# Performance work log

Measured on AMD Instinct MI355X. Metric: run time of the kernel, lower is better.

## Reference

```python
import jax, jax.numpy as jnp
import numpy as np

T, C, O, N = 131072, 512, 512, 1024


def setup_inputs() -> dict:
    key = jax.random.key(0)
    k1, k2, k3, k4, k5 = jax.random.split(key, 5)
    x = jax.random.normal(k1, (T, C), dtype=jnp.float32)
    segment_ids = jnp.sort(jax.random.randint(k2, (T,), 0, N)).astype(jnp.int64)
    # proj_func: Linear(C, O); score_func: Linear(C, 1)
    Wp = jax.random.normal(k3, (C, O), dtype=jnp.float32) / np.sqrt(C)
    bp = jnp.zeros((O,), dtype=jnp.float32)
    ws = jax.random.normal(k4, (C,), dtype=jnp.float32) / np.sqrt(C)
    bs = jnp.zeros((), dtype=jnp.float32)
    return {"x": x, "Wp": Wp, "bp": bp, "ws": ws, "bs": bs,
            "segment_ids": segment_ids, "num_segments": N}


def reference(x, Wp, bp, ws, bs, segment_ids, num_segments):
    # proj_x = Linear(x): [T, O]
    proj_x = x @ Wp + bp
    # score = Linear(x) squeezed to [T]
    score = x @ ws + bs
    # segment-wise numerically stable softmax over ragged segments
    seg_max = jax.ops.segment_max(score, segment_ids, num_segments=num_segments)
    seg_max = jnp.where(jnp.isfinite(seg_max), seg_max, 0.0)  # empty segments
    e = jnp.exp(score - seg_max[segment_ids])
    denom = jax.ops.segment_sum(e, segment_ids, num_segments=num_segments)
    w = e / denom[segment_ids]  # [T]
    # per-segment weighted sum of projected features -> [N, O]
    out = jax.ops.segment_sum(proj_x * w[:, None], segment_ids,
                              num_segments=num_segments)
    return out
```

## Files before the change

### kernel.cpp

```cpp
#include <hip/hip_runtime.h>
#include <hip/hip_bf16.h>
#include <cstdint>
#include <cstddef>

#define CC 512
#define OO 512
#define NN 1024
#define QPARTS 8
#define TB 4

__global__ void seg_bounds_kernel(const int* __restrict__ sid,
                                  int* __restrict__ seg_start,
                                  int T, int N) {
    int t = blockIdx.x * blockDim.x + threadIdx.x;
    if (t >= T) return;
    int s  = sid[t];
    int sp = (t == 0) ? -1 : sid[t - 1];
    for (int n = sp + 1; n <= s; ++n) seg_start[n] = t;
    if (t == T - 1) {
        for (int n = s + 1; n <= N; ++n) seg_start[n] = T;
    }
}

__device__ __forceinline__ float dot4(const float4 a, const float4 b) {
    return a.x * b.x + a.y * b.y + a.z * b.z + a.w * b.w;
}

__global__ __launch_bounds__(64) void seg_pool_partial(
    const float* __restrict__ x,
    const float* __restrict__ ws_g,
    const float* __restrict__ bs_g,
    const int*   __restrict__ seg_start,
    float*       __restrict__ pacc,
    float2*      __restrict__ pml)
{
    const int g = blockIdx.x;
    const int n = g >> 3;
    const int q = g & 7;
    const int s = seg_start[n];
    const int e = seg_start[n + 1];
    const int len = e - s;
    const int tb = s + (len * q) / QPARTS;
    const int te = s + (len * (q + 1)) / QPARTS;
    const int lane = threadIdx.x;
    const int c0 = lane * 4;

    const float4 w0 = *reinterpret_cast<const float4*>(ws_g + c0);
    const float4 w1 = *reinterpret_cast<const float4*>(ws_g + 256 + c0);
    const float  bsv = bs_g[0];

    float m = -INFINITY, l = 0.f;
    float4 a0 = make_float4(0.f, 0.f, 0.f, 0.f);
    float4 a1 = make_float4(0.f, 0.f, 0.f, 0.f);

    float4 A0[TB], A1[TB], B0[TB], B1[TB];

    auto LOADF = [&](float4 (&b0)[TB], float4 (&b1)[TB], const int t0) {
        #pragma unroll
        for (int j = 0; j < TB; ++j) {
            const int t = t0 + j;
            if (t < te) {
                const float* p = x + (size_t)t * CC;
                b0[j] = *reinterpret_cast<const float4*>(p + c0);
                b1[j] = *reinterpret_cast<const float4*>(p + 256 + c0);
            } else {
                b0[j] = make_float4(0.f, 0.f, 0.f, 0.f);
                b1[j] = make_float4(0.f, 0.f, 0.f, 0.f);
            }
        }
    };

    auto COMP = [&](float4 (&b0)[TB], float4 (&b1)[TB], const int t0) {
        float sc[TB];
        #pragma unroll
        for (int j = 0; j < TB; ++j) {
            float p = dot4(b0[j], w0) + dot4(b1[j], w1);
            #pragma unroll
            for (int off = 32; off >= 1; off >>= 1)
                p += __shfl_xor(p, off, 64);
            sc[j] = p + bsv;
        }
        float mc = -INFINITY;
        #pragma unroll
        for (int j = 0; j < TB; ++j)
            if (t0 + j < te) mc = fmaxf(mc, sc[j]);
        if (mc > m) {
            const float scale = (m == -INFINITY) ? 0.f : __expf(m - mc);
            l *= scale;
            a0.x *= scale; a0.y *= scale; a0.z *= scale; a0.w *= scale;
            a1.x *= scale; a1.y *= scale; a1.z *= scale; a1.w *= scale;
            m = mc;
        }
        #pragma unroll
        for (int j = 0; j < TB; ++j) {
            if (t0 + j < te) {
                const float wj = __expf(sc[j] - m);
                l += wj;
                a0.x += wj * b0[j].x; a0.y += wj * b0[j].y;
                a0.z += wj * b0[j].z; a0.w += wj * b0[j].w;
                a1.x += wj * b1[j].x; a1.y += wj * b1[j].y;
                a1.z += wj * b1[j].z; a1.w += wj * b1[j].w;
            }
        }
    };

    LOADF(A0, A1, tb);
    for (int t0 = tb; t0 < te; t0 += 2 * TB) {
        LOADF(B0, B1, t0 + TB);
        COMP(A0, A1, t0);
        LOADF(A0, A1, t0 + 2 * TB);
        COMP(B0, B1, t0 + TB);
    }

    float* pa = pacc + (size_t)g * CC;
    *reinterpret_cast<float4*>(pa + c0)       = a0;
    *reinterpret_cast<float4*>(pa + 256 + c0) = a1;
    if (lane == 0) pml[g] = make_float2(m, l);
}

__global__ __launch_bounds__(64) void seg_combine(
    const float*  __restrict__ pacc,
    const float2* __restrict__ pml,
    float*        __restrict__ y)
{
    const int n = blockIdx.x;
    const int lane = threadIdx.x;
    const int c0 = lane * 4;
    float* yp = y + (size_t)n * CC;

    float mq[QPARTS];
    float lq[QPARTS];
    float newm = -INFINITY;
    #pragma unroll
    for (int q = 0; q < QPARTS; ++q) {
        const float2 ml = pml[n * QPARTS + q];
        mq[q] = ml.x; lq[q] = ml.y;
        newm = fmaxf(newm, ml.x);
    }

    float4 o0 = make_float4(0.f, 0.f, 0.f, 0.f);
    float4 o1 = make_float4(0.f, 0.f, 0.f, 0.f);

    if (newm == -INFINITY) {
        *reinterpret_cast<float4*>(yp + c0)       = o0;
        *reinterpret_cast<float4*>(yp + 256 + c0) = o1;
        return;
    }

    float L = 0.f;
    #pragma unroll
    for (int q = 0; q < QPARTS; ++q) {
        const float wq = __expf(mq[q] - newm);
        L += wq * lq[q];
        const float* pa = pacc + (size_t)(n * QPARTS + q) * CC;
        const float4 p0 = *reinterpret_cast<const float4*>(pa + c0);
        const float4 p1 = *reinterpret_cast<const float4*>(pa + 256 + c0);
        o0.x += wq * p0.x; o0.y += wq * p0.y; o0.z += wq * p0.z; o0.w += wq * p0.w;
        o1.x += wq * p1.x; o1.y += wq * p1.y; o1.z += wq * p1.z; o1.w += wq * p1.w;
    }
    const float inv = 1.f / L;
    o0.x *= inv; o0.y *= inv; o0.z *= inv; o0.w *= inv;
    o1.x *= inv; o1.y *= inv; o1.z *= inv; o1.w *= inv;
    *reinterpret_cast<float4*>(yp + c0)       = o0;
    *reinterpret_cast<float4*>(yp + 256 + c0) = o1;
}

__global__ __launch_bounds__(256) void proj_kernel(
    float*       __restrict__ out,
    const float* __restrict__ Wp,
    const float* __restrict__ bp,
    const int*   __restrict__ seg_start)
{
    const int n0  = blockIdx.x * 4;
    const int tid = threadIdx.x;

    __shared__ float ylds[4][CC];
    {
        const float* src = out + (size_t)n0 * CC;
        for (int idx = tid; idx < 4 * CC / 4; idx += 256)
            reinterpret_cast<float4*>(&ylds[0][0])[idx] =
                reinterpret_cast<const float4*>(src)[idx];
    }
    __syncthreads();

    const int o0 = tid;
    const int o1 = tid + 256;
    float acc[4][2] = {};

    for (int k = 0; k < CC; k += 4) {
        float4 yv[4];
        #pragma unroll
        for (int r = 0; r < 4; ++r)
            yv[r] = *reinterpret_cast<const float4*>(&ylds[r][k]);
        #pragma unroll
        for (int kk = 0; kk < 4; ++kk) {
            const float w0 = Wp[(size_t)(k + kk) * OO + o0];
            const float w1 = Wp[(size_t)(k + kk) * OO + o1];
            #pragma unroll
            for (int r = 0; r < 4; ++r) {
                const float yval = reinterpret_cast<const float*>(&yv[r])[kk];
                acc[r][0] += yval * w0;
                acc[r][1] += yval * w1;
            }
        }
    }

    #pragma unroll
    for (int r = 0; r < 4; ++r) {
        const int n = n0 + r;
        const bool nonempty = seg_start[n + 1] > seg_start[n];
        const float b0 = nonempty ? bp[o0] : 0.f;
        const float b1 = nonempty ? bp[o1] : 0.f;
        out[(size_t)n * OO + o0] = acc[r][0] + b0;
        out[(size_t)n * OO + o1] = acc[r][1] + b1;
    }
}

extern "C" void kernel_launch(void* const* d_in, const int* in_sizes, int n_in,
                              void* d_out, int out_size, void* d_ws, size_t ws_size,
                              hipStream_t stream) {
    const float* x    = (const float*)d_in[0];
    const float* Wp   = (const float*)d_in[1];
    const float* bp   = (const float*)d_in[2];
    const float* wsv  = (const float*)d_in[3];
    const float* bs   = (const float*)d_in[4];
    const int*   sid  = (const int*)d_in[5];
    const int T = in_sizes[5];
    const int N = NN;

    int*    seg_start = (int*)d_ws;
    float*  pacc      = (float*)((char*)d_ws + 8192);
    float2* pml       = (float2*)((char*)d_ws + 8192 +
                                  (size_t)N * QPARTS * CC * sizeof(float));
    float*  out       = (float*)d_out;

    seg_bounds_kernel<<<(T + 255) / 256, 256, 0, stream>>>(sid, seg_start, T, N);
    seg_pool_partial<<<N * QPARTS, 64, 0, stream>>>(x, wsv, bs, seg_start, pacc, pml);
    seg_combine<<<N, 64, 0, stream>>>(pacc, pml, out);
    proj_kernel<<<N / 4, 256, 0, stream>>>(out, Wp, bp, seg_start);
}
```

Measured before the change: 92.05 us.

## Halve segment split count, use nontemporal loads and branchless aligned main loop

Each segment is now split into 4 partial blocks instead of 8, which halves the partial-accumulator traffic and the combine work. Split boundaries are aligned to multiples of 8 tokens, so the double-buffered main loop needs no per-token bounds checks and a separate tail loop handles leftovers. The streaming loads of x use nontemporal hints, and the online-softmax rescale becomes branchless using ext_vector float4 arithmetic. The cost is fewer blocks in flight (4096 single-wave blocks), which may reduce latency hiding on a memory-bound scan of a 256MB input.

```diff
diff --git a/kernel.cpp b/kernel.cpp
--- a/kernel.cpp
+++ b/kernel.cpp
@@ -6,8 +6,9 @@
 #define CC 512
 #define OO 512
 #define NN 1024
-#define QPARTS 8
-#define TB 4
+#define QP 4
+
+typedef float f4 __attribute__((ext_vector_type(4)));
 
 __global__ void seg_bounds_kernel(const int* __restrict__ sid,
                                   int* __restrict__ seg_start,
@@ -22,8 +23,15 @@
     }
 }
 
-__device__ __forceinline__ float dot4(const float4 a, const float4 b) {
+__device__ __forceinline__ float dot4(const f4 a, const f4 b) {
     return a.x * b.x + a.y * b.y + a.z * b.z + a.w * b.w;
+}
+
+__device__ __forceinline__ float wave_sum(float p) {
+    #pragma unroll
+    for (int off = 32; off >= 1; off >>= 1)
+        p += __shfl_xor(p, off, 64);
+    return p;
 }
 
 __global__ __launch_bounds__(64) void seg_pool_partial(
@@ -35,86 +43,113 @@
     float2*      __restrict__ pml)
 {
     const int g = blockIdx.x;
-    const int n = g >> 3;
-    const int q = g & 7;
+    const int n = g >> 2;
+    const int q = g & 3;
     const int s = seg_start[n];
     const int e = seg_start[n + 1];
     const int len = e - s;
-    const int tb = s + (len * q) / QPARTS;
-    const int te = s + (len * (q + 1)) / QPARTS;
+    const int tb = s + (((len * q) >> 2) & ~7);
+    const int te = (q == 3) ? e : (s + (((len * (q + 1)) >> 2) & ~7));
     const int lane = threadIdx.x;
     const int c0 = lane * 4;
 
-    const float4 w0 = *reinterpret_cast<const float4*>(ws_g + c0);
-    const float4 w1 = *reinterpret_cast<const float4*>(ws_g + 256 + c0);
-    const float  bsv = bs_g[0];
+    const f4 w0 = *reinterpret_cast<const f4*>(ws_g + c0);
+    const f4 w1 = *reinterpret_cast<const f4*>(ws_g + 256 + c0);
+    const float bsv = bs_g[0];
 
     float m = -INFINITY, l = 0.f;
-    float4 a0 = make_float4(0.f, 0.f, 0.f, 0.f);
-    float4 a1 = make_float4(0.f, 0.f, 0.f, 0.f);
-
-    float4 A0[TB], A1[TB], B0[TB], B1[TB];
-
-    auto LOADF = [&](float4 (&b0)[TB], float4 (&b1)[TB], const int t0) {
-        #pragma unroll
-        for (int j = 0; j < TB; ++j) {
-            const int t = t0 + j;
-            if (t < te) {
-                const float* p = x + (size_t)t * CC;
-                b0[j] = *reinterpret_cast<const float4*>(p + c0);
-                b1[j] = *reinterpret_cast<const float4*>(p + 256 + c0);
-            } else {
-                b0[j] = make_float4(0.f, 0.f, 0.f, 0.f);
-                b1[j] = make_float4(0.f, 0.f, 0.f, 0.f);
-            }
+    f4 a0 = {0.f, 0.f, 0.f, 0.f};
+    f4 a1 = {0.f, 0.f, 0.f, 0.f};
+
+    const int nTok  = te - tb;
+    const int nIter = nTok >> 3;
+
+    f4 A0[4], A1[4], B0[4], B1[4];
+
+    auto LOAD4 = [&](f4 (&b0)[4], f4 (&b1)[4], const float* p) {
+        #pragma unroll
+        for (int j = 0; j < 4; ++j) {
+            const float* r = p + (size_t)j * CC;
+            b0[j] = __builtin_nontemporal_load(
+                        reinterpret_cast<const f4*>(r + c0));
+            b1[j] = __builtin_nontemporal_load(
+                        reinterpret_cast<const f4*>(r + 256 + c0));
         }
     };
 
-    auto COMP = [&](float4 (&b0)[TB], float4 (&b1)[TB], const int t0) {
-        float sc[TB];
-        #pragma unroll
-        for (int j = 0; j < TB; ++j) {
-            float p = dot4(b0[j], w0) + dot4(b1[j], w1);
-            #pragma unroll
-            for (int off = 32; off >= 1; off >>= 1)
-                p += __shfl_xor(p, off, 64);
-            sc[j] = p + bsv;
-        }
-        float mc = -INFINITY;
-        #pragma unroll
-        for (int j = 0; j < TB; ++j)
-            if (t0 + j < te) mc = fmaxf(mc, sc[j]);
-        if (mc > m) {
-            const float scale = (m == -INFINITY) ? 0.f : __expf(m - mc);
-            l *= scale;
-            a0.x *= scale; a0.y *= scale; a0.z *= scale; a0.w *= scale;
-            a1.x *= scale; a1.y *= scale; a1.z *= scale; a1.w *= scale;
-            m = mc;
-        }
-        #pragma unroll
-        for (int j = 0; j < TB; ++j) {
-            if (t0 + j < te) {
-                const float wj = __expf(sc[j] - m);
-                l += wj;
-                a0.x += wj * b0[j].x; a0.y += wj * b0[j].y;
-                a0.z += wj * b0[j].z; a0.w += wj * b0[j].w;
-                a1.x += wj * b1[j].x; a1.y += wj * b1[j].y;
-                a1.z += wj * b1[j].z; a1.w += wj * b1[j].w;
-            }
+    auto COMP4 = [&](const f4 (&b0)[4], const f4 (&b1)[4]) {
+        float sc[4];
+        #pragma unroll
+        for (int j = 0; j < 4; ++j)
+            sc[j] = wave_sum(dot4(b0[j], w0) + dot4(b1[j], w1)) + bsv;
+        const float mc = fmaxf(fmaxf(sc[0], sc[1]), fmaxf(sc[2], sc[3]));
+        const float newm  = fmaxf(m, mc);
+        const float scale = __expf(m - newm);
+        m = newm;
+        l *= scale;
+        a0 *= scale;
+        a1 *= scale;
+        #pragma unroll
+        for (int j = 0; j < 4; ++j) {
+            const float wj = __expf(sc[j] - m);
+            l += wj;
+            a0 += wj * b0[j];
+            a1 += wj * b1[j];
         }
     };
 
-    LOADF(A0, A1, tb);
-    for (int t0 = tb; t0 < te; t0 += 2 * TB) {
-        LOADF(B0, B1, t0 + TB);
-        COMP(A0, A1, t0);
-        LOADF(A0, A1, t0 + 2 * TB);
-        COMP(B0, B1, t0 + TB);
+    const float* base = x + (size_t)tb * CC;
+
+    if (nIter > 0) {
+        LOAD4(A0, A1, base);
+        for (int i = 0; i < nIter - 1; ++i) {
+            const float* p = base + (size_t)(i * 8) * CC;
+            LOAD4(B0, B1, p + 4 * CC);
+            COMP4(A0, A1);
+            LOAD4(A0, A1, p + 8 * CC);
+            COMP4(B0, B1);
+        }
+        LOAD4(B0, B1, base + (size_t)((nIter - 1) * 8 + 4) * CC);
+        COMP4(A0, A1);
+        COMP4(B0, B1);
+    }
+
+    for (int t0 = tb + nIter * 8; t0 < te; t0 += 4) {
+        #pragma unroll
+        for (int j = 0; j < 4; ++j) {
+            int t = t0 + j;
+            t = (t < te) ? t : (te - 1);
+            const float* r = x + (size_t)t * CC;
+            A0[j] = __builtin_nontemporal_load(
+                        reinterpret_cast<const f4*>(r + c0));
+            A1[j] = __builtin_nontemporal_load(
+                        reinterpret_cast<const f4*>(r + 256 + c0));
+        }
+        float sc[4];
+        #pragma unroll
+        for (int j = 0; j < 4; ++j) {
+            sc[j] = wave_sum(dot4(A0[j], w0) + dot4(A1[j], w1)) + bsv;
+            if (t0 + j >= te) sc[j] = -INFINITY;
+        }
+        const float mc = fmaxf(fmaxf(sc[0], sc[1]), fmaxf(sc[2], sc[3]));
+        const float newm  = fmaxf(m, mc);
+        const float scale = __expf(m - newm);
+        m = newm;
+        l *= scale;
+        a0 *= scale;
+        a1 *= scale;
+        #pragma unroll
+        for (int j = 0; j < 4; ++j) {
+            const float wj = __expf(sc[j] - m);
+            l += wj;
+            a0 += wj * A0[j];
+            a1 += wj * A1[j];
+        }
     }
 
     float* pa = pacc + (size_t)g * CC;
-    *reinterpret_cast<float4*>(pa + c0)       = a0;
-    *reinterpret_cast<float4*>(pa + 256 + c0) = a1;
+    *reinterpret_cast<f4*>(pa + c0)       = a0;
+    *reinterpret_cast<f4*>(pa + 256 + c0) = a1;
     if (lane == 0) pml[g] = make_float2(m, l);
 }
 
@@ -128,41 +163,40 @@
     const int c0 = lane * 4;
     float* yp = y + (size_t)n * CC;
 
-    float mq[QPARTS];
-    float lq[QPARTS];
+    float mq[QP], lq[QP];
     float newm = -INFINITY;
     #pragma unroll
-    for (int q = 0; q < QPARTS; ++q) {
-        const float2 ml = pml[n * QPARTS + q];
+    for (int q = 0; q < QP; ++q) {
+        const float2 ml = pml[n * QP + q];
         mq[q] = ml.x; lq[q] = ml.y;
         newm = fmaxf(newm, ml.x);
     }
 
-    float4 o0 = make_float4(0.f, 0.f, 0.f, 0.f);
-    float4 o1 = make_float4(0.f, 0.f, 0.f, 0.f);
+    f4 o0 = {0.f, 0.f, 0.f, 0.f};
+    f4 o1 = {0.f, 0.f, 0.f, 0.f};
 
     if (newm == -INFINITY) {
-        *reinterpret_cast<float4*>(yp + c0)       = o0;
-        *reinterpret_cast<float4*>(yp + 256 + c0) = o1;
+        *reinterpret_cast<f4*>(yp + c0)       = o0;
+        *reinterpret_cast<f4*>(yp + 256 + c0) = o1;
         return;
     }
 
     float L = 0.f;
     #pragma unroll
-    for (int q = 0; q < QPARTS; ++q) {
+    for (int q = 0; q < QP; ++q) {
         const float wq = __expf(mq[q] - newm);
         L += wq * lq[q];
-        const float* pa = pacc + (size_t)(n * QPARTS + q) * CC;
-        const float4 p0 = *reinterpret_cast<const float4*>(pa + c0);
-        const float4 p1 = *reinterpret_cast<const float4*>(pa + 256 + c0);
-        o0.x += wq * p0.x; o0.y += wq * p0.y; o0.z += wq * p0.z; o0.w += wq * p0.w;
-        o1.x += wq * p1.x; o1.y += wq * p1.y; o1.z += wq * p1.z; o1.w += wq * p1.w;
+        const float* pa = pacc + (size_t)(n * QP + q) * CC;
+        const f4 p0 = *reinterpret_cast<const f4*>(pa + c0);
+        const f4 p1 = *reinterpret_cast<const f4*>(pa + 256 + c0);
+        o0 += wq * p0;
+        o1 += wq * p1;
     }
     const float inv = 1.f / L;
-    o0.x *= inv; o0.y *= inv; o0.z *= inv; o0.w *= inv;
-    o1.x *= inv; o1.y *= inv; o1.z *= inv; o1.w *= inv;
-    *reinterpret_cast<float4*>(yp + c0)       = o0;
-    *reinterpret_cast<float4*>(yp + 256 + c0) = o1;
+    o0 *= inv;
+    o1 *= inv;
+    *reinterpret_cast<f4*>(yp + c0)       = o0;
+    *reinterpret_cast<f4*>(yp + 256 + c0) = o1;
 }
 
 __global__ __launch_bounds__(256) void proj_kernel(
@@ -231,11 +265,11 @@
     int*    seg_start = (int*)d_ws;
     float*  pacc      = (float*)((char*)d_ws + 8192);
     float2* pml       = (float2*)((char*)d_ws + 8192 +
-                                  (size_t)N * QPARTS * CC * sizeof(float));
+                                  (size_t)N * QP * CC * sizeof(float));
     float*  out       = (float*)d_out;
 
     seg_bounds_kernel<<<(T + 255) / 256, 256, 0, stream>>>(sid, seg_start, T, N);
-    seg_pool_partial<<<N * QPARTS, 64, 0, stream>>>(x, wsv, bs, seg_start, pacc, pml);
+    seg_pool_partial<<<N * QP, 64, 0, stream>>>(x, wsv, bs, seg_start, pacc, pml);
     seg_combine<<<N, 64, 0, stream>>>(pacc, pml, out);
     proj_kernel<<<N / 4, 256, 0, stream>>>(out, Wp, bp, seg_start);
 }
```

After: 89.85 us. 2.4% less time.
